# Kernel tuning notes

Hardware: AMD Instinct MI355X
Metric: run time of the kernel (lower is better)

The kernel has to match this reference:

```python
import jax, jax.numpy as jnp
import numpy as np

EMBED = 1024
NUM_EXPERTS = 8
TOP_K = 2


def setup_inputs() -> dict:
    key = jax.random.key(0)
    ks = jax.random.split(key, 6)
    scale = EMBED ** -0.5  # keep activations numerically sane
    return {
        "x": jax.random.normal(ks[0], (4, 4096, EMBED), jnp.float32),
        "router_w": jax.random.normal(ks[1], (EMBED, NUM_EXPERTS), jnp.float32) * scale,
        "router_b": jnp.zeros((NUM_EXPERTS,), jnp.float32),
        "we_gate": jax.random.normal(ks[2], (NUM_EXPERTS, EMBED, EMBED), jnp.float32) * scale,
        "we_up": jax.random.normal(ks[3], (NUM_EXPERTS, EMBED, EMBED), jnp.float32) * scale,
        "we_down": jax.random.normal(ks[4], (NUM_EXPERTS, EMBED, EMBED), jnp.float32) * scale,
    }


def reference(x, router_w, router_b, we_gate, we_up, we_down):
    x_shape = x.shape
    x_flat = x.reshape(-1, x_shape[-1])            # [T, D]
    num_tokens = x_flat.shape[0]

    router_logits = x_flat @ router_w + router_b    # [T, E]
    topk_weights, topk_indices = jax.lax.top_k(router_logits, k=TOP_K)
    topk_weights = jax.nn.softmax(topk_weights, axis=-1)  # [T, K]

    token_idx_mesh = jnp.repeat(jnp.arange(num_tokens), TOP_K)  # [T*K]
    expert_idx_mesh = topk_indices.reshape(-1)                  # [T*K]

    sort_permutation = jnp.argsort(expert_idx_mesh)  # stable sort by expert
    sorted_expert_idx = expert_idx_mesh[sort_permutation]
    sorted_token_idx = token_idx_mesh[sort_permutation]
    group_sizes = jnp.bincount(sorted_expert_idx, length=NUM_EXPERTS)

    sorted_tokens = x_flat[sorted_token_idx]  # [T*K, D] gather (ragged dispatch)

    ff_gate = jax.lax.ragged_dot(sorted_tokens, we_gate, group_sizes)  # [T*K, D]
    ff_up = jax.lax.ragged_dot(sorted_tokens, we_up, group_sizes)      # [T*K, D]
    activated = jax.nn.silu(ff_gate) * ff_up
    ff_out = jax.lax.ragged_dot(activated, we_down, group_sizes)       # [T*K, D]

    # fuse router weighting into the combine (scatter-add) step
    sorted_weights = topk_weights.reshape(-1)[sort_permutation]  # [T*K]
    ff_out = ff_out * sorted_weights[:, None]

    output_flat = jnp.zeros_like(x_flat).at[sorted_token_idx].add(ff_out)
    return output_flat.reshape(x_shape)
```

## Files before the change

### kernel.cpp

```cpp
#include <hip/hip_runtime.h>
#include <hip/hip_bf16.h>
#include <cstdint>
#include <cstddef>

typedef unsigned short u16;
typedef unsigned int u32;
typedef __attribute__((ext_vector_type(8))) short short8;
typedef __attribute__((ext_vector_type(4))) float floatx4;

#define DD 1024
#define NE 8

#define GLOAD_LDS16(G, L)                                               \
  __builtin_amdgcn_global_load_lds(                                     \
      (const __attribute__((address_space(1))) void*)(G),               \
      (__attribute__((address_space(3))) void*)(L), 16, 0, 0)

#define LDSA(P) ((u32)(uintptr_t)(const __attribute__((address_space(3))) void*)(P))

#define DSR(DST, ADDR, IMM)                                             \
  asm volatile("ds_read_b128 %0, %1 offset:" IMM : "=v"(DST) : "v"(ADDR))

__device__ __forceinline__ u16 f2bf(float f) {
  union { __hip_bfloat16 h; u16 u; } cv;
  cv.h = __float2bfloat16(f);
  return cv.u;
}

__device__ __forceinline__ float2 bf2f2(u32 u) {
  union { u32 v; float f; } lo, hi;
  lo.v = u << 16; hi.v = u & 0xffff0000u;
  float2 r; r.x = lo.f; r.y = hi.f; return r;
}

__global__ __launch_bounds__(256) void router_kernel(
    const float* __restrict__ x, const float* __restrict__ rw,
    const float* __restrict__ rb, int2* __restrict__ experts,
    float2* __restrict__ wts, u16* __restrict__ xbf, int T) {
  const int wave = threadIdx.x >> 6;
  const int lane = threadIdx.x & 63;
  const int t = blockIdx.x * 4 + wave;
  if (t >= T) return;
  const float* xr = x + (size_t)t * DD;
  float acc[NE] = {0.f, 0.f, 0.f, 0.f, 0.f, 0.f, 0.f, 0.f};
#pragma unroll
  for (int i = 0; i < 16; i++) {
    const int idx = lane + i * 64;
    const float xv = xr[idx];
    xbf[(size_t)t * DD + idx] = f2bf(xv);
    const float4* r4 = (const float4*)(rw + (size_t)idx * NE);
    float4 a = r4[0], b = r4[1];
    acc[0] += xv * a.x; acc[1] += xv * a.y; acc[2] += xv * a.z; acc[3] += xv * a.w;
    acc[4] += xv * b.x; acc[5] += xv * b.y; acc[6] += xv * b.z; acc[7] += xv * b.w;
  }
#pragma unroll
  for (int s = 1; s < 64; s <<= 1)
#pragma unroll
    for (int e = 0; e < NE; e++)
      acc[e] += __shfl_xor(acc[e], s);
  if (lane == 0) {
    float lg[NE];
#pragma unroll
    for (int e = 0; e < NE; e++) lg[e] = acc[e] + rb[e];
    float l0 = lg[0]; int i0 = 0;
#pragma unroll
    for (int e = 1; e < NE; e++) if (lg[e] > l0) { l0 = lg[e]; i0 = e; }
    float l1 = -3.4e38f; int i1 = 0;
#pragma unroll
    for (int e = 0; e < NE; e++) {
      if (e == i0) continue;
      if (lg[e] > l1) { l1 = lg[e]; i1 = e; }
    }
    const float w0 = 1.f / (1.f + expf(l1 - l0));
    experts[t] = make_int2(i0, i1);
    wts[t] = make_float2(w0, 1.f - w0);
  }
}

__global__ __launch_bounds__(256) void count_kernel(
    const int2* __restrict__ experts, int* __restrict__ counts, int T) {
  __shared__ int lc[NE];
  if (threadIdx.x < NE) lc[threadIdx.x] = 0;
  __syncthreads();
  const int t = blockIdx.x * 256 + threadIdx.x;
  if (t < T) {
    int2 e = experts[t];
    atomicAdd(&lc[e.x], 1);
    atomicAdd(&lc[e.y], 1);
  }
  __syncthreads();
  if (threadIdx.x < NE && lc[threadIdx.x] > 0)
    atomicAdd(&counts[threadIdx.x], lc[threadIdx.x]);
}

__global__ void offsets_kernel(const int* __restrict__ counts, int* __restrict__ offsets) {
  int s = 0;
  for (int e = 0; e < NE; e++) { offsets[e] = s; s += counts[e]; }
}

__global__ __launch_bounds__(256) void scatter_kernel(
    const int2* __restrict__ experts, const int* __restrict__ offsets,
    int* __restrict__ cursors, int* __restrict__ tok_id,
    int2* __restrict__ slots, int T) {
  __shared__ int lc[NE], lb[NE];
  if (threadIdx.x < NE) lc[threadIdx.x] = 0;
  __syncthreads();
  const int t = blockIdx.x * 256 + threadIdx.x;
  int2 e = make_int2(0, 0);
  int p0 = 0, p1 = 0;
  if (t < T) {
    e = experts[t];
    p0 = atomicAdd(&lc[e.x], 1);
    p1 = atomicAdd(&lc[e.y], 1);
  }
  __syncthreads();
  if (threadIdx.x < NE) lb[threadIdx.x] = atomicAdd(&cursors[threadIdx.x], lc[threadIdx.x]);
  __syncthreads();
  if (t < T) {
    const int s0 = offsets[e.x] + lb[e.x] + p0;
    const int s1 = offsets[e.y] + lb[e.y] + p1;
    tok_id[s0] = t;
    tok_id[s1] = t;
    slots[t] = make_int2(s0, s1);
  }
}

__global__ __launch_bounds__(256) void convert_kernel(
    const float* __restrict__ wg, const float* __restrict__ wu,
    const float* __restrict__ wd, u16* __restrict__ Wgu, u16* __restrict__ Wd) {
  const int z = blockIdx.z;
  const int mat = z >> 3;
  const int e = z & 7;
  const float* src = (mat == 0 ? wg : (mat == 1 ? wu : wd)) + (size_t)e * DD * DD;
  __shared__ float tile[64][65];
  const int k0 = blockIdx.y * 64, n0 = blockIdx.x * 64;
  const int tx = threadIdx.x & 63, ty = threadIdx.x >> 6;
#pragma unroll
  for (int i = 0; i < 16; i++) {
    const int kk = i * 4 + ty;
    tile[kk][tx] = src[(size_t)(k0 + kk) * DD + n0 + tx];
  }
  __syncthreads();
#pragma unroll
  for (int i = 0; i < 16; i++) {
    const int nn = i * 4 + ty;
    const int n = n0 + nn;
    const u16 h = f2bf(tile[tx][nn]);
    if (mat == 2) {
      Wd[((size_t)e * DD + n) * DD + k0 + tx] = h;
    } else {
      const int nc = ((n >> 3) << 4) | (mat << 3) | (n & 7);
      Wgu[((size_t)e * 2048 + nc) * DD + k0 + tx] = h;
    }
  }
}


#define STAGE(BUF, KOFF)                                                \
  {                                                                     \
    _Pragma("unroll")                                                   \
    for (int i = 0; i < 4; i++) {                                       \
      GLOAD_LDS16(srcA[i] + (KOFF), &As[(BUF) * 8192 + t * 8 + i * 2048]); \
      GLOAD_LDS16(srcB[i] + (KOFF), &Bs[(BUF) * 8192 + t * 8 + i * 2048]); \
    }                                                                   \
  }

#define COMPUTE(BUF)                                                    \
  {                                                                     \
    _Pragma("unroll")                                                   \
    for (int s = 0; s < 2; s++) {                                       \
      short8 a[4], b[4];                                                \
      const u32 ab_ = asb + (u32)(BUF) * 16384u + offA + cks[s];        \
      const u32 bb_ = bsb + (u32)(BUF) * 16384u + offB + cks[s];        \
      DSR(a[0], ab_, "0");    DSR(a[1], ab_, "2048");                   \
      DSR(a[2], ab_, "4096"); DSR(a[3], ab_, "6144");                   \
      DSR(b[0], bb_, "0");    DSR(b[1], bb_, "2048");                   \
      DSR(b[2], bb_, "4096"); DSR(b[3], bb_, "6144");                   \
      asm volatile("s_waitcnt lgkmcnt(0)");                             \
      __builtin_amdgcn_sched_barrier(0);                                \
      __builtin_amdgcn_s_setprio(1);                                    \
      _Pragma("unroll")                                                 \
      for (int i = 0; i < 4; i++)                                       \
        _Pragma("unroll")                                               \
        for (int j = 0; j < 4; j++)                                     \
          acc[i][j] = __builtin_amdgcn_mfma_f32_16x16x32_bf16(          \
              a[i], b[j], acc[i][j], 0, 0, 0);                          \
      __builtin_amdgcn_s_setprio(0);                                    \
      __builtin_amdgcn_sched_barrier(0);                                \
    }                                                                   \
  }

#define SYNC0()                                                         \
  __builtin_amdgcn_sched_barrier(0);                                    \
  asm volatile("s_waitcnt vmcnt(0)");                                   \
  __builtin_amdgcn_s_barrier();                                         \
  __builtin_amdgcn_sched_barrier(0);

#define GEMM128_LOOP()                                                  \
  STAGE(0, 0);                                                          \
  SYNC0();                                                              \
  int cur = 0;                                                          \
  _Pragma("unroll 1")                                                   \
  for (int kk = 0; kk < 15; ++kk) {                                     \
    STAGE(cur ^ 1, (kk + 1) * 64);                                      \
    COMPUTE(cur);                                                       \
    SYNC0();                                                            \
    cur ^= 1;                                                           \
  }                                                                     \
  COMPUTE(cur);

__global__ __launch_bounds__(256, 2) void gateup_kernel(
    const u16* __restrict__ xbf, const u16* __restrict__ Wgu,
    const int* __restrict__ tok_id, const int* __restrict__ offsets,
    const int* __restrict__ counts, u16* __restrict__ H) {
  const int e = blockIdx.z;
  const int cnt = counts[e];
  const int m0 = blockIdx.y * 128;
  if (m0 >= cnt) return;
  const int off = offsets[e];
  const int n0 = blockIdx.x * 128;

  __shared__ u16 As[2 * 8192];
  __shared__ u16 Bs[2 * 8192];

  const int t = threadIdx.x;
  const int lane = t & 63;
  const int wave = t >> 6;
  const int wm = (wave >> 1) * 64;
  const int wn = (wave & 1) * 64;
  const int r16 = lane & 15;
  const int quad = lane >> 4;
  const u32 offA = (u32)((wm + r16) * 128);
  const u32 offB = (u32)((wn + r16) * 128);
  u32 cks[2];
  cks[0] = (u32)(((quad) ^ (r16 & 7)) * 16);
  cks[1] = (u32)(((4 + quad) ^ (r16 & 7)) * 16);
  const u32 asb = LDSA(&As[0]);
  const u32 bsb = LDSA(&Bs[0]);

  const int drow = t >> 3;
  const int dpos = t & 7;
  const u16* srcA[4];
  const u16* srcB[4];
  const u16* bbase = Wgu + ((size_t)e * 2048 + n0) * DD;
#pragma unroll
  for (int i = 0; i < 4; i++) {
    const int row = drow + i * 32;
    int r = m0 + row; if (r > cnt - 1) r = cnt - 1;
    const int tok = tok_id[off + r];
    const int ka = (dpos ^ (row & 7)) * 8;
    srcA[i] = xbf + (size_t)tok * DD + ka;
    srcB[i] = bbase + (size_t)row * DD + ka;
  }

  floatx4 acc[4][4];
#pragma unroll
  for (int i = 0; i < 4; i++)
#pragma unroll
    for (int j = 0; j < 4; j++)
      acc[i][j] = (floatx4){0.f, 0.f, 0.f, 0.f};

  GEMM128_LOOP();

#pragma unroll
  for (int i = 0; i < 4; i++) {
    const int mb = m0 + wm + i * 16 + quad * 4;
#pragma unroll
    for (int j = 0; j < 4; j++) {
      const int nc = n0 + wn + j * 16 + r16;
      const int ng = ((nc >> 4) << 3) | (nc & 7);
#pragma unroll
      for (int r = 0; r < 4; r++) {
        const float v = acc[i][j][r];
        const float pv = __shfl_xor(v, 8);
        const float g = (lane & 8) ? pv : v;
        const float u = (lane & 8) ? v : pv;
        const float hv = g * u / (1.f + __expf(-g));
        const int m = mb + r;
        if (!(lane & 8) && m < cnt)
          H[(size_t)(off + m) * DD + ng] = f2bf(hv);
      }
    }
  }
}

__global__ __launch_bounds__(256, 2) void down_kernel(
    const u16* __restrict__ H, const u16* __restrict__ Wd,
    const int* __restrict__ counts, const int* __restrict__ offsets,
    u16* __restrict__ Y, int TK2) {
  const int e = blockIdx.z;
  const int cnt = counts[e];
  const int m0 = blockIdx.y * 128;
  if (m0 >= cnt) return;
  const int off = offsets[e];
  const int n0 = blockIdx.x * 128;

  __shared__ u16 As[2 * 8192];
  __shared__ u16 Bs[2 * 8192];

  const int t = threadIdx.x;
  const int lane = t & 63;
  const int wave = t >> 6;
  const int wm = (wave >> 1) * 64;
  const int wn = (wave & 1) * 64;
  const int r16 = lane & 15;
  const int quad = lane >> 4;
  const u32 offA = (u32)((wm + r16) * 128);
  const u32 offB = (u32)((wn + r16) * 128);
  u32 cks[2];
  cks[0] = (u32)(((quad) ^ (r16 & 7)) * 16);
  cks[1] = (u32)(((4 + quad) ^ (r16 & 7)) * 16);
  const u32 asb = LDSA(&As[0]);
  const u32 bsb = LDSA(&Bs[0]);

  const int drow = t >> 3;
  const int dpos = t & 7;
  const u16* srcA[4];
  const u16* srcB[4];
  const u16* bbase = Wd + ((size_t)e * DD + n0) * DD;
#pragma unroll
  for (int i = 0; i < 4; i++) {
    const int row = drow + i * 32;
    int r = off + m0 + row; if (r > TK2 - 1) r = TK2 - 1;
    const int ka = (dpos ^ (row & 7)) * 8;
    srcA[i] = H + (size_t)r * DD + ka;
    srcB[i] = bbase + (size_t)row * DD + ka;
  }

  floatx4 acc[4][4];
#pragma unroll
  for (int i = 0; i < 4; i++)
#pragma unroll
    for (int j = 0; j < 4; j++)
      acc[i][j] = (floatx4){0.f, 0.f, 0.f, 0.f};

  GEMM128_LOOP();

#pragma unroll
  for (int i = 0; i < 4; i++) {
    const int mb = m0 + wm + i * 16 + quad * 4;
#pragma unroll
    for (int r = 0; r < 4; r++) {
      const int m = mb + r;
      if (m < cnt) {
        u16* yrow = Y + (size_t)(off + m) * DD + n0 + wn + r16;
#pragma unroll
        for (int j = 0; j < 4; j++)
          yrow[j * 16] = f2bf(acc[i][j][r]);
      }
    }
  }
}

#undef STAGE
#undef COMPUTE
#undef SYNC0

__global__ __launch_bounds__(256) void combine_kernel(
    const u16* __restrict__ Y, const int2* __restrict__ slots,
    const float2* __restrict__ wts, float* __restrict__ out, int T) {
  const int wave = threadIdx.x >> 6;
  const int lane = threadIdx.x & 63;
  const int t = blockIdx.x * 4 + wave;
  if (t >= T) return;
  const int2 s = slots[t];
  const float2 w = wts[t];
  const uint4* y0 = (const uint4*)(Y + (size_t)s.x * DD);
  const uint4* y1 = (const uint4*)(Y + (size_t)s.y * DD);
  float4* o = (float4*)(out + (size_t)t * DD);
#pragma unroll
  for (int c = 0; c < 2; c++) {
    const int idx = lane + c * 64;
    const uint4 a = y0[idx];
    const uint4 b = y1[idx];
    const u32 au[4] = {a.x, a.y, a.z, a.w};
    const u32 bu[4] = {b.x, b.y, b.z, b.w};
    float4 r[2];
#pragma unroll
    for (int q = 0; q < 4; q++) {
      const float2 fa = bf2f2(au[q]);
      const float2 fb = bf2f2(bu[q]);
      ((float*)r)[q * 2]     = w.x * fa.x + w.y * fb.x;
      ((float*)r)[q * 2 + 1] = w.x * fa.y + w.y * fb.y;
    }
    o[idx * 2]     = r[0];
    o[idx * 2 + 1] = r[1];
  }
}

extern "C" void kernel_launch(void* const* d_in, const int* in_sizes, int n_in,
                              void* d_out, int out_size, void* d_ws, size_t ws_size,
                              hipStream_t stream) {
  const float* x  = (const float*)d_in[0];
  const float* rw = (const float*)d_in[1];
  const float* rb = (const float*)d_in[2];
  const float* wg = (const float*)d_in[3];
  const float* wu = (const float*)d_in[4];
  const float* wd = (const float*)d_in[5];
  float* out = (float*)d_out;
  const int T = in_sizes[0] / DD;
  const int TK2 = 2 * T;

  char* p = (char*)d_ws;
  int* ctrl = (int*)p; p += 256;
  int2* experts = (int2*)p;  p += (size_t)T * 8;
  float2* wtsp  = (float2*)p; p += (size_t)T * 8;
  int* tok_id   = (int*)p;   p += (size_t)TK2 * 4;
  int2* slots   = (int2*)p;  p += (size_t)T * 8;
  u16* Wd       = (u16*)p;   p += (size_t)NE * DD * DD * 2;
  u16* H        = (u16*)p;   p += (size_t)TK2 * DD * 2;
  u16* Wgu      = (u16*)p;
  u16* xbf      = (u16*)(p + (size_t)NE * 2048 * DD * 2);
  u16* Y        = (u16*)p;
  p += (size_t)TK2 * DD * 2;
  if ((size_t)(p - (char*)d_ws) > ws_size) return;

  hipMemsetAsync(ctrl, 0, 256, stream);

  router_kernel<<<T / 4, 256, 0, stream>>>(x, rw, rb, experts, wtsp, xbf, T);
  count_kernel<<<T / 256, 256, 0, stream>>>(experts, ctrl, T);
  offsets_kernel<<<1, 1, 0, stream>>>(ctrl, ctrl + 16);
  scatter_kernel<<<T / 256, 256, 0, stream>>>(experts, ctrl + 16, ctrl + 8, tok_id, slots, T);
  convert_kernel<<<dim3(16, 16, 24), 256, 0, stream>>>(wg, wu, wd, Wgu, Wd);
  gateup_kernel<<<dim3(16, (T + 127) / 128, NE), 256, 0, stream>>>(
      xbf, Wgu, tok_id, ctrl + 16, ctrl, H);
  down_kernel<<<dim3(8, (T + 127) / 128, NE), 256, 0, stream>>>(
      H, Wd, ctrl, ctrl + 16, Y, TK2);
  combine_kernel<<<T / 4, 256, 0, stream>>>(Y, slots, wtsp, out, T);
}
```

Measured before the change: 529.2 us.

## Overlap next-stage global loads with compute via partial vmcnt wait and batched LDS reads

Restructures the GEMM main loop so each K-step waits only for the current buffer's global-to-LDS loads (vmcnt(8)) instead of draining all outstanding loads. The prefetch for the next buffer can then stay in flight during compute. It also issues all 16 LDS reads for both k-substeps before the MFMAs, which removes one lgkmcnt wait per step. A second barrier after compute guards buffer reuse. The cost is higher register pressure from holding 16 short8 fragments, under launch bounds that target 2 blocks per CU.

Result: faster. 516.7 us (-2.4%).

```diff
diff --git a/kernel.cpp b/kernel.cpp
--- a/kernel.cpp
+++ b/kernel.cpp
@@ -165,49 +165,57 @@
     }                                                                   \
   }
 
-#define COMPUTE(BUF)                                                    \
+#define KSTEP(VM)                                                       \
   {                                                                     \
+    __builtin_amdgcn_sched_barrier(0);                                  \
+    asm volatile("s_waitcnt vmcnt(" VM ")");                            \
+    __builtin_amdgcn_s_barrier();                                       \
+    __builtin_amdgcn_sched_barrier(0);                                  \
+    short8 a0[4], b0[4], a1[4], b1[4];                                  \
+    const u32 base_ = (u32)cur * 16384u;                                \
+    const u32 a0_ = asb + base_ + offA + cks0;                          \
+    const u32 b0_ = bsb + base_ + offB + cks0;                          \
+    const u32 a1_ = asb + base_ + offA + cks1;                          \
+    const u32 b1_ = bsb + base_ + offB + cks1;                          \
+    DSR(a0[0], a0_, "0");    DSR(a0[1], a0_, "2048");                   \
+    DSR(a0[2], a0_, "4096"); DSR(a0[3], a0_, "6144");                   \
+    DSR(b0[0], b0_, "0");    DSR(b0[1], b0_, "2048");                   \
+    DSR(b0[2], b0_, "4096"); DSR(b0[3], b0_, "6144");                   \
+    DSR(a1[0], a1_, "0");    DSR(a1[1], a1_, "2048");                   \
+    DSR(a1[2], a1_, "4096"); DSR(a1[3], a1_, "6144");                   \
+    DSR(b1[0], b1_, "0");    DSR(b1[1], b1_, "2048");                   \
+    DSR(b1[2], b1_, "4096"); DSR(b1[3], b1_, "6144");                   \
+    asm volatile("s_waitcnt lgkmcnt(0)");                               \
+    __builtin_amdgcn_sched_barrier(0);                                  \
+    __builtin_amdgcn_s_setprio(1);                                      \
     _Pragma("unroll")                                                   \
-    for (int s = 0; s < 2; s++) {                                       \
-      short8 a[4], b[4];                                                \
-      const u32 ab_ = asb + (u32)(BUF) * 16384u + offA + cks[s];        \
-      const u32 bb_ = bsb + (u32)(BUF) * 16384u + offB + cks[s];        \
-      DSR(a[0], ab_, "0");    DSR(a[1], ab_, "2048");                   \
-      DSR(a[2], ab_, "4096"); DSR(a[3], ab_, "6144");                   \
-      DSR(b[0], bb_, "0");    DSR(b[1], bb_, "2048");                   \
-      DSR(b[2], bb_, "4096"); DSR(b[3], bb_, "6144");                   \
-      asm volatile("s_waitcnt lgkmcnt(0)");                             \
-      __builtin_amdgcn_sched_barrier(0);                                \
-      __builtin_amdgcn_s_setprio(1);                                    \
+    for (int i = 0; i < 4; i++)                                         \
       _Pragma("unroll")                                                 \
-      for (int i = 0; i < 4; i++)                                       \
-        _Pragma("unroll")                                               \
-        for (int j = 0; j < 4; j++)                                     \
-          acc[i][j] = __builtin_amdgcn_mfma_f32_16x16x32_bf16(          \
-              a[i], b[j], acc[i][j], 0, 0, 0);                          \
-      __builtin_amdgcn_s_setprio(0);                                    \
-      __builtin_amdgcn_sched_barrier(0);                                \
-    }                                                                   \
-  }
-
-#define SYNC0()                                                         \
-  __builtin_amdgcn_sched_barrier(0);                                    \
-  asm volatile("s_waitcnt vmcnt(0)");                                   \
-  __builtin_amdgcn_s_barrier();                                         \
-  __builtin_amdgcn_sched_barrier(0);
+      for (int j = 0; j < 4; j++)                                       \
+        acc[i][j] = __builtin_amdgcn_mfma_f32_16x16x32_bf16(            \
+            a0[i], b0[j], acc[i][j], 0, 0, 0);                          \
+    _Pragma("unroll")                                                   \
+    for (int i = 0; i < 4; i++)                                         \
+      _Pragma("unroll")                                                 \
+      for (int j = 0; j < 4; j++)                                       \
+        acc[i][j] = __builtin_amdgcn_mfma_f32_16x16x32_bf16(            \
+            a1[i], b1[j], acc[i][j], 0, 0, 0);                          \
+    __builtin_amdgcn_s_setprio(0);                                      \
+    __builtin_amdgcn_sched_barrier(0);                                  \
+    __builtin_amdgcn_s_barrier();                                       \
+    __builtin_amdgcn_sched_barrier(0);                                  \
+  }
 
 #define GEMM128_LOOP()                                                  \
   STAGE(0, 0);                                                          \
-  SYNC0();                                                              \
   int cur = 0;                                                          \
   _Pragma("unroll 1")                                                   \
   for (int kk = 0; kk < 15; ++kk) {                                     \
     STAGE(cur ^ 1, (kk + 1) * 64);                                      \
-    COMPUTE(cur);                                                       \
-    SYNC0();                                                            \
+    KSTEP("8");                                                         \
     cur ^= 1;                                                           \
   }                                                                     \
-  COMPUTE(cur);
+  KSTEP("0");
 
 __global__ __launch_bounds__(256, 2) void gateup_kernel(
     const u16* __restrict__ xbf, const u16* __restrict__ Wgu,
@@ -232,9 +240,8 @@
   const int quad = lane >> 4;
   const u32 offA = (u32)((wm + r16) * 128);
   const u32 offB = (u32)((wn + r16) * 128);
-  u32 cks[2];
-  cks[0] = (u32)(((quad) ^ (r16 & 7)) * 16);
-  cks[1] = (u32)(((4 + quad) ^ (r16 & 7)) * 16);
+  const u32 cks0 = (u32)(((quad) ^ (r16 & 7)) * 16);
+  const u32 cks1 = (u32)(((4 + quad) ^ (r16 & 7)) * 16);
   const u32 asb = LDSA(&As[0]);
   const u32 bsb = LDSA(&Bs[0]);
 
@@ -307,9 +314,8 @@
   const int quad = lane >> 4;
   const u32 offA = (u32)((wm + r16) * 128);
   const u32 offB = (u32)((wn + r16) * 128);
-  u32 cks[2];
-  cks[0] = (u32)(((quad) ^ (r16 & 7)) * 16);
-  cks[1] = (u32)(((4 + quad) ^ (r16 & 7)) * 16);
+  const u32 cks0 = (u32)(((quad) ^ (r16 & 7)) * 16);
+  const u32 cks1 = (u32)(((4 + quad) ^ (r16 & 7)) * 16);
   const u32 asb = LDSA(&As[0]);
   const u32 bsb = LDSA(&Bs[0]);
 
@@ -353,8 +359,7 @@
 }
 
 #undef STAGE
-#undef COMPUTE
-#undef SYNC0
+#undef KSTEP
 
 __global__ __launch_bounds__(256) void combine_kernel(
     const u16* __restrict__ Y, const int2* __restrict__ slots,
```
